# Performance work log

Hardware: AMD Instinct MI355X
Metric: run time of the kernel (lower is better)

The kernel has to match this reference:

```python
import jax, jax.numpy as jnp
import numpy as np

PALACE_N = 64   # base palace mask size
PALACE_BLOCK = 8  # 8 palaces of 8 positions each


def _palace_base():
    # base 64x64 mask: 1.0 within a palace (8x8 diagonal blocks), 0.5 across palaces
    pid = jnp.arange(PALACE_N) // PALACE_BLOCK
    intra = pid[:, None] == pid[None, :]
    return jnp.where(intra, 1.0, 0.5).astype(jnp.float32)


def _get_mask(T, inter_palace_weight):
    # tile base mask by index modulo 64 (matches mask[i % 64, j % 64])
    base = _palace_base()
    ii = jnp.arange(T) % PALACE_N
    base_T = base[ii[:, None], ii[None, :]]            # [T, T]
    intra = (base_T == 1.0).astype(jnp.float32)
    inter = (base_T < 1.0).astype(jnp.float32)
    return intra + jax.nn.sigmoid(inter_palace_weight) * inter


def setup_inputs() -> dict:
    key = jax.random.key(0)
    ks = jax.random.split(key, 5)
    B, T, D = 4, 2048, 1024
    x = jax.random.normal(ks[0], (B, T, D), dtype=jnp.float32)
    s = 1.0 / np.sqrt(D)
    Wq = jax.random.normal(ks[1], (D, D), dtype=jnp.float32) * s
    Wk = jax.random.normal(ks[2], (D, D), dtype=jnp.float32) * s
    Wv = jax.random.normal(ks[3], (D, D), dtype=jnp.float32) * s
    inter_palace_weight = jnp.float32(0.1)
    return {"x": x, "Wq": Wq, "Wk": Wk, "Wv": Wv,
            "inter_palace_weight": inter_palace_weight}


def reference(x, Wq, Wk, Wv, inter_palace_weight):
    B, T, D = x.shape
    H = 16
    hd = D // H
    scale = hd ** -0.5
    pmask = _get_mask(T, inter_palace_weight)          # [T, T]
    # torch Linear: x @ W.T
    q = (x @ Wq.T).reshape(B, T, H, hd)
    k = (x @ Wk.T).reshape(B, T, H, hd)
    v = (x @ Wv.T).reshape(B, T, H, hd)
    attn = jnp.einsum('bqhd,bkhd->bhqk', q, k) * scale
    attn = attn * pmask[None, None, :, :]
    attn = jax.nn.softmax(attn, axis=-1)
    attn = jnp.nan_to_num(attn, nan=0.0)
    out = jnp.einsum('bhqk,bkhd->bqhd', attn, v)
    return out.reshape(B, T, D)
```

## Files before the change

### kernel.cpp

```cpp
#include <hip/hip_runtime.h>

typedef unsigned short u16;
typedef unsigned int u32;
typedef short bf16x8 __attribute__((ext_vector_type(8)));
typedef float f32x4 __attribute__((ext_vector_type(4)));
typedef u32 u32x4 __attribute__((ext_vector_type(4)));

#define AS_GLOBAL __attribute__((address_space(1)))
#define AS_LDS __attribute__((address_space(3)))

__device__ __forceinline__ void async16(const void* g, void* l) {
  __builtin_amdgcn_global_load_lds((const AS_GLOBAL u32*)g, (AS_LDS u32*)l, 16, 0, 0);
}

__device__ __forceinline__ u16 f2bf(float f) {
  u32 u = __builtin_bit_cast(u32, f);
  u += 0x7FFFu + ((u >> 16) & 1u);
  return (u16)(u >> 16);
}

__device__ __forceinline__ u32 pk2bf(float lo, float hi) {
  return __builtin_amdgcn_perm(__builtin_bit_cast(u32, hi),
                               __builtin_bit_cast(u32, lo), 0x07060302u);
}

__device__ __forceinline__ float fexp2(float x) {
#if __has_builtin(__builtin_amdgcn_exp2f)
  return __builtin_amdgcn_exp2f(x);
#else
  return exp2f(x);
#endif
}

__global__ __launch_bounds__(256) void cvt_all(const float* __restrict__ x,
                                               const float* __restrict__ wq,
                                               const float* __restrict__ wk,
                                               const float* __restrict__ wv,
                                               u16* __restrict__ xb,
                                               u16* __restrict__ wb) {
  const int blk = blockIdx.x;
  const float* src;
  u16* dst;
  int i;
  if (blk < 8192) {
    src = x; dst = xb; i = blk * 256 + threadIdx.x;
  } else if (blk < 9216) {
    src = wq; dst = wb; i = (blk - 8192) * 256 + threadIdx.x;
  } else if (blk < 10240) {
    src = wk; dst = wb + 1048576; i = (blk - 9216) * 256 + threadIdx.x;
  } else {
    src = wv; dst = wb + 2097152; i = (blk - 10240) * 256 + threadIdx.x;
  }
  float4 f = reinterpret_cast<const float4*>(src)[i];
  ushort4 o;
  o.x = f2bf(f.x); o.y = f2bf(f.y); o.z = f2bf(f.z); o.w = f2bf(f.w);
  reinterpret_cast<ushort4*>(dst)[i] = o;
}

__global__ __launch_bounds__(256, 2) void qkv_gemm(const u16* __restrict__ X,
                                                   const u16* __restrict__ W,
                                                   u16* __restrict__ O) {
  const int z = blockIdx.z;
  const u16* Wz = W + (size_t)z * (1024 * 1024);
  u16* Oz = O + (size_t)z * (8192 * 1024);

  __shared__ __align__(16) u16 As[2][128 * 64];
  __shared__ __align__(16) u16 Bs[2][128 * 64];

  const int t = threadIdx.x;
  const int lane = t & 63, w = t >> 6, quad = lane >> 4, lq = lane & 15;
  const int wm = (w >> 1) * 64, wn = (w & 1) * 64;
  const int sw = lq & 7;
  const size_t m0 = (size_t)blockIdx.x * 128;
  const int n0 = blockIdx.y * 128;

  int off[4];
#pragma unroll
  for (int j = 0; j < 4; ++j) {
    const int s = j * 256 + t, row = s >> 3, c = (s & 7) ^ (row & 7);
    off[j] = row * 1024 + c * 8;
  }
  const u16* gA = X + m0 * 1024;
  const u16* gB = Wz + (size_t)n0 * 1024;

  f32x4 acc[4][4];
#pragma unroll
  for (int i = 0; i < 4; ++i)
#pragma unroll
    for (int j = 0; j < 4; ++j) acc[i][j] = f32x4{0.f, 0.f, 0.f, 0.f};

  auto stage = [&](int kt, int nb) {
    const u16* ga = gA + kt * 64;
    const u16* gb = gB + kt * 64;
#pragma unroll
    for (int j = 0; j < 4; ++j)
      async16(ga + off[j], &As[nb][(j * 256 + t) * 8]);
#pragma unroll
    for (int j = 0; j < 4; ++j)
      async16(gb + off[j], &Bs[nb][(j * 256 + t) * 8]);
  };

  stage(0, 0);

  for (int kt = 0; kt < 16; ++kt) {
    const int cur = kt & 1;
    __syncthreads();
    if (kt < 15) stage(kt + 1, cur ^ 1);

    bf16x8 Af[4][2], Bf[4][2];
#pragma unroll
    for (int i = 0; i < 4; ++i)
#pragma unroll
      for (int ks = 0; ks < 2; ++ks) {
        Af[i][ks] = *reinterpret_cast<const bf16x8*>(
            &As[cur][(wm + i * 16 + lq) * 64 + ((ks * 4 + quad) ^ sw) * 8]);
        Bf[i][ks] = *reinterpret_cast<const bf16x8*>(
            &Bs[cur][(wn + i * 16 + lq) * 64 + ((ks * 4 + quad) ^ sw) * 8]);
      }
#pragma unroll
    for (int i = 0; i < 4; ++i)
#pragma unroll
      for (int j = 0; j < 4; ++j) {
        acc[i][j] = __builtin_amdgcn_mfma_f32_16x16x32_bf16(Af[i][0], Bf[j][0], acc[i][j], 0, 0, 0);
        acc[i][j] = __builtin_amdgcn_mfma_f32_16x16x32_bf16(Af[i][1], Bf[j][1], acc[i][j], 0, 0, 0);
      }
  }

#pragma unroll
  for (int i = 0; i < 4; ++i) {
#pragma unroll
    for (int j = 0; j < 4; ++j) {
      const int n = n0 + wn + j * 16 + lq;
      const int hh = n >> 6, d = n & 63;
#pragma unroll
      for (int r = 0; r < 4; ++r) {
        const size_t m = m0 + wm + i * 16 + quad * 4 + r;
        const size_t bb = m >> 11, tt = m & 2047;
        if (z != 2)
          Oz[((bb * 16 + hh) * 2048 + tt) * 64 + d] = f2bf(acc[i][j][r]);
        else
          Oz[((bb * 16 + hh) * 64 + d) * 2048 + tt] = f2bf(acc[i][j][r]);
      }
    }
  }
}

__global__ __launch_bounds__(256, 2) void palace_attn(const u16* __restrict__ Q,
                                                      const u16* __restrict__ K,
                                                      const u16* __restrict__ Vt,
                                                      float* __restrict__ out,
                                                      const float* __restrict__ wptr) {
  const int bh = blockIdx.x, qt = blockIdx.y;
  const int h = bh & 15, b = bh >> 4;
  const size_t base = (size_t)bh * (2048 * 64);

  __shared__ __align__(16) u16 Ks[2][64 * 64];
  __shared__ __align__(16) u16 Vs[2][64 * 64];

  const int t = threadIdx.x;
  const int w = t >> 6, lane = t & 63, quad = lane >> 4, lq = lane & 15;
  const int lq3 = lq >> 3;
  const int swk = (lq & 3) | (((lq >> 2) & 1) << 2);
  const int swv = (lq & 3) | (lq3 << 2);
  const float sig = 1.f / (1.f + __expf(-wptr[0]));
  const float Ci = 0.125f * 1.44269504f;
  const float Co = Ci * sig;
  const float MC = 14.4269504f;

  float cft[2][4];
#pragma unroll
  for (int half = 0; half < 2; ++half)
#pragma unroll
    for (int qg = 0; qg < 4; ++qg)
      cft[half][qg] = (half * 4 + quad == qg * 2 + lq3) ? Ci : Co;

  bf16x8 qf[4][2];
#pragma unroll
  for (int qg = 0; qg < 4; ++qg)
#pragma unroll
    for (int kc = 0; kc < 2; ++kc)
      qf[qg][kc] = *reinterpret_cast<const bf16x8*>(
          Q + base + (size_t)(qt * 256 + w * 64 + qg * 16 + lq) * 64 + kc * 32 + quad * 8);

  int ko[2], vo[2];
#pragma unroll
  for (int r = 0; r < 2; ++r) {
    const int slot = r * 256 + t;
    const int row = slot >> 3;
    const int sr = (row & 3) | (((row >> 3) & 1) << 2);
    const int cl = (slot & 7) ^ sr;
    ko[r] = row * 64 + cl * 8;
    vo[r] = row * 2048 + cl * 8;
  }

  f32x4 O[4][4];
  f32x4 Lacc[4];
#pragma unroll
  for (int qg = 0; qg < 4; ++qg) {
    Lacc[qg] = f32x4{0.f, 0.f, 0.f, 0.f};
#pragma unroll
    for (int dg = 0; dg < 4; ++dg) O[qg][dg] = f32x4{0.f, 0.f, 0.f, 0.f};
  }

  const short oneb = (short)0x3F80;
  const bf16x8 ones8 = {oneb, oneb, oneb, oneb, oneb, oneb, oneb, oneb};

  {
    const u16* kgp = K + base;
    const u16* vgp = Vt + base;
    async16(kgp + ko[0], &Ks[0][(w * 64) * 8]);
    async16(kgp + ko[1], &Ks[0][(256 + w * 64) * 8]);
    async16(vgp + vo[0], &Vs[0][(w * 64) * 8]);
    async16(vgp + vo[1], &Vs[0][(256 + w * 64) * 8]);
  }

  for (int kt = 0; kt < 32; ++kt) {
    const int cur = kt & 1;
    __syncthreads();
    if (kt < 31) {
      const u16* kgp = K + base + (size_t)(kt + 1) * 4096;
      const u16* vgp = Vt + base + (size_t)(kt + 1) * 64;
      const int nb = cur ^ 1;
      async16(kgp + ko[0], &Ks[nb][(w * 64) * 8]);
      async16(kgp + ko[1], &Ks[nb][(256 + w * 64) * 8]);
      async16(vgp + vo[0], &Vs[nb][(w * 64) * 8]);
      async16(vgp + vo[1], &Vs[nb][(256 + w * 64) * 8]);
    }

#pragma unroll
    for (int half = 0; half < 2; ++half) {
      const int rb = half * 32 + ((lq >> 2) << 3) + (lq & 3);
      bf16x8 kf[2][2];
#pragma unroll
      for (int kg2 = 0; kg2 < 2; ++kg2) {
        const int krow = rb + kg2 * 4;
        kf[kg2][0] = *reinterpret_cast<const bf16x8*>(
            &Ks[cur][krow * 64 + (quad ^ swk) * 8]);
        kf[kg2][1] = *reinterpret_cast<const bf16x8*>(
            &Ks[cur][krow * 64 + ((quad + 4) ^ swk) * 8]);
      }

      bf16x8 vbf[4];
#pragma unroll
      for (int dg = 0; dg < 4; ++dg)
        vbf[dg] = *reinterpret_cast<const bf16x8*>(
            &Vs[cur][(dg * 16 + lq) * 64 + ((half * 4 + quad) ^ swv) * 8]);

#pragma unroll
      for (int qg = 0; qg < 4; ++qg) {
        f32x4 z0 = {0.f, 0.f, 0.f, 0.f}, z1 = {0.f, 0.f, 0.f, 0.f};
        z0 = __builtin_amdgcn_mfma_f32_16x16x32_bf16(kf[0][0], qf[qg][0], z0, 0, 0, 0);
        z0 = __builtin_amdgcn_mfma_f32_16x16x32_bf16(kf[0][1], qf[qg][1], z0, 0, 0, 0);
        z1 = __builtin_amdgcn_mfma_f32_16x16x32_bf16(kf[1][0], qf[qg][0], z1, 0, 0, 0);
        z1 = __builtin_amdgcn_mfma_f32_16x16x32_bf16(kf[1][1], qf[qg][1], z1, 0, 0, 0);

        const float cf = cft[half][qg];
        const float p0 = fexp2(__builtin_fmaf(z0[0], cf, -MC));
        const float p1 = fexp2(__builtin_fmaf(z0[1], cf, -MC));
        const float p2 = fexp2(__builtin_fmaf(z0[2], cf, -MC));
        const float p3 = fexp2(__builtin_fmaf(z0[3], cf, -MC));
        const float p4 = fexp2(__builtin_fmaf(z1[0], cf, -MC));
        const float p5 = fexp2(__builtin_fmaf(z1[1], cf, -MC));
        const float p6 = fexp2(__builtin_fmaf(z1[2], cf, -MC));
        const float p7 = fexp2(__builtin_fmaf(z1[3], cf, -MC));

        u32x4 pk;
        pk.x = pk2bf(p0, p1);
        pk.y = pk2bf(p2, p3);
        pk.z = pk2bf(p4, p5);
        pk.w = pk2bf(p6, p7);
        const bf16x8 pa = __builtin_bit_cast(bf16x8, pk);

        Lacc[qg] = __builtin_amdgcn_mfma_f32_16x16x32_bf16(pa, ones8, Lacc[qg], 0, 0, 0);
#pragma unroll
        for (int dg = 0; dg < 4; ++dg)
          O[qg][dg] = __builtin_amdgcn_mfma_f32_16x16x32_bf16(pa, vbf[dg], O[qg][dg], 0, 0, 0);
      }
    }
  }

#pragma unroll
  for (int qg = 0; qg < 4; ++qg) {
#pragma unroll
    for (int r = 0; r < 4; ++r) {
      const float iv = 1.f / Lacc[qg][r];
      const size_t trow = (size_t)(qt * 256 + w * 64 + qg * 16 + quad * 4 + r);
      float* op = out + ((size_t)b * 2048 + trow) * 1024 + h * 64 + lq;
#pragma unroll
      for (int dg = 0; dg < 4; ++dg) op[dg * 16] = O[qg][dg][r] * iv;
    }
  }
}

extern "C" void kernel_launch(void* const* d_in, const int* in_sizes, int n_in,
                              void* d_out, int out_size, void* d_ws, size_t ws_size,
                              hipStream_t stream) {
  (void)in_sizes; (void)n_in; (void)out_size; (void)ws_size;
  const float* x = (const float*)d_in[0];
  const float* Wq = (const float*)d_in[1];
  const float* Wk = (const float*)d_in[2];
  const float* Wv = (const float*)d_in[3];
  const float* wip = (const float*)d_in[4];
  float* out = (float*)d_out;

  u16* xb = (u16*)d_ws;
  u16* wb = xb + 8388608;
  u16* qb = wb + 3145728;
  u16* kb = qb + 8388608;
  u16* vb = kb + 8388608;

  cvt_all<<<11264, 256, 0, stream>>>(x, Wq, Wk, Wv, xb, wb);
  qkv_gemm<<<dim3(64, 8, 3), 256, 0, stream>>>(xb, wb, qb);
  palace_attn<<<dim3(64, 8, 1), 256, 0, stream>>>(qb, kb, vb, out, wip);
}
```

Measured before the change: 246.9 us.

## Deepen QKV GEMM pipeline to 4-stage K=32 tiles with block remap

Replaces the double-buffered K=64 staging in the QKV projection GEMM with a four-buffer K=32 ring that keeps three tiles of async global-to-LDS loads in flight. Waiting on vmcnt replaces full __syncthreads drains. The block index is also remapped so neighbouring workgroups share A/B tiles in L2, and the LDS swizzle is adjusted to the narrower tile. This is meant to hide global load latency and improve cache reuse, at the cost of more barriers per unit of compute and reliance on exact vmcnt accounting.

```diff
diff --git a/kernel.cpp b/kernel.cpp
--- a/kernel.cpp
+++ b/kernel.cpp
@@ -60,24 +60,29 @@
 __global__ __launch_bounds__(256, 2) void qkv_gemm(const u16* __restrict__ X,
                                                    const u16* __restrict__ W,
                                                    u16* __restrict__ O) {
-  const int z = blockIdx.z;
-  const u16* Wz = W + (size_t)z * (1024 * 1024);
-  u16* Oz = O + (size_t)z * (8192 * 1024);
-
-  __shared__ __align__(16) u16 As[2][128 * 64];
-  __shared__ __align__(16) u16 Bs[2][128 * 64];
+  const int orig = blockIdx.x + 64 * (blockIdx.y + (blockIdx.z << 3));
+  const int l = (orig & 7) * 192 + (orig >> 3);
+  const int bx = l & 63;
+  const int by = (l >> 6) & 7;
+  const int bz = l >> 9;
+
+  const u16* Wz = W + (size_t)bz * (1024 * 1024);
+  u16* Oz = O + (size_t)bz * (8192 * 1024);
+
+  __shared__ __align__(16) u16 As[4][128 * 32];
+  __shared__ __align__(16) u16 Bs[4][128 * 32];
 
   const int t = threadIdx.x;
   const int lane = t & 63, w = t >> 6, quad = lane >> 4, lq = lane & 15;
   const int wm = (w >> 1) * 64, wn = (w & 1) * 64;
-  const int sw = lq & 7;
-  const size_t m0 = (size_t)blockIdx.x * 128;
-  const int n0 = blockIdx.y * 128;
-
-  int off[4];
-#pragma unroll
-  for (int j = 0; j < 4; ++j) {
-    const int s = j * 256 + t, row = s >> 3, c = (s & 7) ^ (row & 7);
+  const int swr = (lq >> 1) & 3;
+  const size_t m0 = (size_t)bx * 128;
+  const int n0 = by * 128;
+
+  int off[2];
+#pragma unroll
+  for (int j = 0; j < 2; ++j) {
+    const int s = j * 256 + t, row = s >> 2, c = (s & 3) ^ ((row >> 1) & 3);
     off[j] = row * 1024 + c * 8;
   }
   const u16* gA = X + m0 * 1024;
@@ -90,41 +95,49 @@
     for (int j = 0; j < 4; ++j) acc[i][j] = f32x4{0.f, 0.f, 0.f, 0.f};
 
   auto stage = [&](int kt, int nb) {
-    const u16* ga = gA + kt * 64;
-    const u16* gb = gB + kt * 64;
-#pragma unroll
-    for (int j = 0; j < 4; ++j)
-      async16(ga + off[j], &As[nb][(j * 256 + t) * 8]);
-#pragma unroll
-    for (int j = 0; j < 4; ++j)
-      async16(gb + off[j], &Bs[nb][(j * 256 + t) * 8]);
+    const u16* ga = gA + kt * 32;
+    const u16* gb = gB + kt * 32;
+    async16(ga + off[0], &As[nb][t * 8]);
+    async16(ga + off[1], &As[nb][(256 + t) * 8]);
+    async16(gb + off[0], &Bs[nb][t * 8]);
+    async16(gb + off[1], &Bs[nb][(256 + t) * 8]);
   };
 
+  auto compute_tile = [&](int cur) {
+    bf16x8 Af[4], Bf[4];
+#pragma unroll
+    for (int i = 0; i < 4; ++i) {
+      Af[i] = *reinterpret_cast<const bf16x8*>(
+          &As[cur][(wm + i * 16 + lq) * 32 + (quad ^ swr) * 8]);
+      Bf[i] = *reinterpret_cast<const bf16x8*>(
+          &Bs[cur][(wn + i * 16 + lq) * 32 + (quad ^ swr) * 8]);
+    }
+#pragma unroll
+    for (int i = 0; i < 4; ++i)
+#pragma unroll
+      for (int j = 0; j < 4; ++j)
+        acc[i][j] = __builtin_amdgcn_mfma_f32_16x16x32_bf16(Af[i], Bf[j], acc[i][j], 0, 0, 0);
+  };
+
   stage(0, 0);
-
-  for (int kt = 0; kt < 16; ++kt) {
-    const int cur = kt & 1;
-    __syncthreads();
-    if (kt < 15) stage(kt + 1, cur ^ 1);
-
-    bf16x8 Af[4][2], Bf[4][2];
-#pragma unroll
-    for (int i = 0; i < 4; ++i)
-#pragma unroll
-      for (int ks = 0; ks < 2; ++ks) {
-        Af[i][ks] = *reinterpret_cast<const bf16x8*>(
-            &As[cur][(wm + i * 16 + lq) * 64 + ((ks * 4 + quad) ^ sw) * 8]);
-        Bf[i][ks] = *reinterpret_cast<const bf16x8*>(
-            &Bs[cur][(wn + i * 16 + lq) * 64 + ((ks * 4 + quad) ^ sw) * 8]);
-      }
-#pragma unroll
-    for (int i = 0; i < 4; ++i)
-#pragma unroll
-      for (int j = 0; j < 4; ++j) {
-        acc[i][j] = __builtin_amdgcn_mfma_f32_16x16x32_bf16(Af[i][0], Bf[j][0], acc[i][j], 0, 0, 0);
-        acc[i][j] = __builtin_amdgcn_mfma_f32_16x16x32_bf16(Af[i][1], Bf[j][1], acc[i][j], 0, 0, 0);
-      }
-  }
+  stage(1, 1);
+  stage(2, 2);
+
+  for (int kt = 0; kt < 30; ++kt) {
+    asm volatile("s_waitcnt vmcnt(8)" ::: "memory");
+    __builtin_amdgcn_s_barrier();
+    __builtin_amdgcn_sched_barrier(0);
+    if (kt < 29) stage(kt + 3, (kt + 3) & 3);
+    compute_tile(kt & 3);
+  }
+  asm volatile("s_waitcnt vmcnt(4)" ::: "memory");
+  __builtin_amdgcn_s_barrier();
+  __builtin_amdgcn_sched_barrier(0);
+  compute_tile(2);
+  asm volatile("s_waitcnt vmcnt(0)" ::: "memory");
+  __builtin_amdgcn_s_barrier();
+  __builtin_amdgcn_sched_barrier(0);
+  compute_tile(3);
 
 #pragma unroll
   for (int i = 0; i < 4; ++i) {
@@ -136,7 +149,7 @@
       for (int r = 0; r < 4; ++r) {
         const size_t m = m0 + wm + i * 16 + quad * 4 + r;
         const size_t bb = m >> 11, tt = m & 2047;
-        if (z != 2)
+        if (bz != 2)
           Oz[((bb * 16 + hh) * 2048 + tt) * 64 + d] = f2bf(acc[i][j][r]);
         else
           Oz[((bb * 16 + hh) * 64 + d) * 2048 + tt] = f2bf(acc[i][j][r]);
```

Result: slower. 279.2 us (+13.1%).
